# Kernel tuning notes

Hardware: AMD Instinct MI355X
Metric: run time of the kernel (lower is better)

Reference implementation:

```python
import jax, jax.numpy as jnp
import numpy as np

B, S, C = 16, 2048, 1024
H = 8            # preference_dim / num_heads
HD = C // H      # head_dim = 128


def setup_inputs() -> dict:
    key = jax.random.key(0)
    ks = jax.random.split(key, 8)
    s1 = 1.0 / np.sqrt(1.0)   # Linear(1, HD) init scale (not critical)
    sh = 1.0 / np.sqrt(HD)
    return {
        "features": jax.random.normal(ks[0], (B, S, C), dtype=jnp.float32),
        "preference": jax.random.normal(ks[1], (B, H), dtype=jnp.float32),
        "Wq": jax.random.uniform(ks[2], (HD, 1), jnp.float32, -s1, s1),
        "bq": jax.random.uniform(ks[3], (HD,), jnp.float32, -s1, s1),
        "Wk": jax.random.uniform(ks[4], (HD, HD), jnp.float32, -sh, sh),
        "bk": jax.random.uniform(ks[5], (HD,), jnp.float32, -sh, sh),
        "Wv": jax.random.uniform(ks[6], (HD, HD), jnp.float32, -sh, sh),
        "bv": jax.random.uniform(ks[7], (HD,), jnp.float32, -sh, sh),
    }


def reference(features, preference, Wq, bq, Wk, bk, Wv, bv):
    b, s, c = features.shape
    h, hd = H, HD
    # query: Linear(1->hd) applied to per-head scalar preference; constant over step
    # q[b,h,d] = preference[b,h] * Wq[d,0] + bq[d]
    q = preference[:, :, None] * Wq[:, 0][None, None, :] + bq  # [B,H,HD]
    f = features.reshape(b, s, h, hd)                          # head slices
    k = jnp.einsum('bshd,ed->bshe', f, Wk) + bk                # [B,S,H,HD]
    v = jnp.einsum('bshd,ed->bshe', f, Wv) + bv                # [B,S,H,HD]
    # original builds [B,S,S] scores per head, but query rows are identical
    # across step, so softmax(q @ k^T) @ v has identical rows; compute once.
    scores = jnp.einsum('bhd,bshd->bhs', q, k)                 # [B,H,S]
    attn = jax.nn.softmax(scores, axis=-1)
    ctx = jnp.einsum('bhs,bshd->bhd', attn, v)                 # [B,H,HD]
    weighted = jnp.broadcast_to(ctx[:, None, :, :], (b, s, h, hd)).reshape(b, s, c)
    return weighted + features
```

## Files before the change

kernel.cpp:

```cpp
#include <hip/hip_runtime.h>
#include <math.h>

#define B 16
#define S 2048
#define C 1024
#define H 8
#define HD 128

__global__ void k1_qk(const float* __restrict__ pref, const float* __restrict__ Wq,
                      const float* __restrict__ bq, const float* __restrict__ Wk,
                      float* __restrict__ qk) {
    int bh = blockIdx.x;
    int d  = threadIdx.x;
    __shared__ float qsh[HD];
    float p = pref[bh];
    qsh[d] = p * Wq[d] + bq[d];
    __syncthreads();
    float s = 0.f;
#pragma unroll 8
    for (int e = 0; e < HD; ++e)
        s += qsh[e] * Wk[e * HD + d];
    qk[bh * HD + d] = s;
}

__global__ __launch_bounds__(256) void k2_pass(
    const float* __restrict__ feat, const float* __restrict__ qk,
    float* __restrict__ pm, float* __restrict__ pl, float* __restrict__ pf,
    int NC, int R) {
    int wg    = blockIdx.x;
    int b     = wg / NC;
    int chunk = wg - b * NC;
    int t     = threadIdx.x;
    int h     = t >> 5;
    int lane32 = t & 31;

    const float4* frow = (const float4*)feat
                       + (size_t)(b * S + chunk * R) * (C / 4) + t;
    float4 qv = ((const float4*)qk)[(b * H + h) * (HD / 4) + lane32];

    float m = -1e30f, l = 0.f;
    float a0 = 0.f, a1 = 0.f, a2 = 0.f, a3 = 0.f;

    for (int s = 0; s < R; ++s) {
        float4 f = frow[(size_t)s * (C / 4)];
        float part = f.x * qv.x + f.y * qv.y + f.z * qv.z + f.w * qv.w;
        part += __shfl_xor(part, 16, 32);
        part += __shfl_xor(part, 8, 32);
        part += __shfl_xor(part, 4, 32);
        part += __shfl_xor(part, 2, 32);
        part += __shfl_xor(part, 1, 32);
        float mn    = fmaxf(m, part);
        float scale = __expf(m - mn);
        float p     = __expf(part - mn);
        l  = l * scale + p;
        a0 = a0 * scale + p * f.x;
        a1 = a1 * scale + p * f.y;
        a2 = a2 * scale + p * f.z;
        a3 = a3 * scale + p * f.w;
        m  = mn;
    }
    if (lane32 == 0) { pm[wg * H + h] = m; pl[wg * H + h] = l; }
    float4 o; o.x = a0; o.y = a1; o.z = a2; o.w = a3;
    ((float4*)pf)[(size_t)wg * (C / 4) + t] = o;
}

__global__ __launch_bounds__(128) void k3_combine(
    const float* __restrict__ pm, const float* __restrict__ pl,
    const float* __restrict__ pf, const float* __restrict__ Wv,
    const float* __restrict__ bv, float* __restrict__ ctx, int NC) {
    int bh = blockIdx.x;
    int b = bh >> 3, h = bh & 7;
    int t = threadIdx.x;
    __shared__ float wsh[64];
    __shared__ float fsh[HD];

    float M = -1e30f;
    for (int i = 0; i < NC; ++i)
        M = fmaxf(M, pm[(b * NC + i) * H + h]);
    if (t < NC) wsh[t] = __expf(pm[(b * NC + t) * H + h] - M);
    __syncthreads();
    float L = 0.f;
    for (int i = 0; i < NC; ++i)
        L += pl[(b * NC + i) * H + h] * wsh[i];
    float acc = 0.f;
    for (int i = 0; i < NC; ++i)
        acc += pf[(size_t)(b * NC + i) * C + h * HD + t] * wsh[i];
    fsh[t] = acc / L;
    __syncthreads();
    float s = 0.f;
#pragma unroll 8
    for (int d = 0; d < HD; ++d)
        s += fsh[d] * Wv[t * HD + d];
    ctx[bh * HD + t] = s + bv[t];
}

__global__ __launch_bounds__(256) void k4_epilogue(
    const float* __restrict__ feat, const float* __restrict__ ctx,
    float* __restrict__ out) {
    size_t i = (size_t)blockIdx.x * blockDim.x + threadIdx.x;
    float4 f = ((const float4*)feat)[i];
    size_t b  = i >> 19;
    size_t c4 = i & 255;
    float4 cv = ((const float4*)ctx)[b * (C / 4) + c4];
    float4 o; o.x = f.x + cv.x; o.y = f.y + cv.y;
    o.z = f.z + cv.z; o.w = f.w + cv.w;
    ((float4*)out)[i] = o;
}

extern "C" void kernel_launch(void* const* d_in, const int* in_sizes, int n_in,
                              void* d_out, int out_size, void* d_ws, size_t ws_size,
                              hipStream_t stream) {
    const float* feat = (const float*)d_in[0];
    const float* pref = (const float*)d_in[1];
    const float* Wq   = (const float*)d_in[2];
    const float* bq   = (const float*)d_in[3];
    const float* Wk   = (const float*)d_in[4];
    const float* Wv   = (const float*)d_in[6];
    const float* bv   = (const float*)d_in[7];
    float* out = (float*)d_out;

    int NC = 64;
    auto need = [](int nc) {
        return (size_t)(B * H * HD + B * C + 2 * B * nc * H + (size_t)B * nc * C) * 4;
    };
    while (NC > 1 && need(NC) > ws_size) NC >>= 1;
    int R = S / NC;

    float* ws  = (float*)d_ws;
    float* qk  = ws;
    float* ctx = qk + B * H * HD;
    float* pm  = ctx + B * C;
    float* pl  = pm + B * NC * H;
    float* pf  = pl + B * NC * H;

    k1_qk<<<B * H, HD, 0, stream>>>(pref, Wq, bq, Wk, qk);
    k2_pass<<<B * NC, 256, 0, stream>>>(feat, qk, pm, pl, pf, NC, R);
    k3_combine<<<B * H, HD, 0, stream>>>(pm, pl, pf, Wv, bv, ctx, NC);
    k4_epilogue<<<(B * S * C / 4) / 256, 256, 0, stream>>>(feat, ctx, out);
}
```

Baseline: 292.0 us.

## Use lazy max rescaling in online softmax, transpose Wv, nontemporal epilogue stores

The streaming softmax pass now rescales the running max and accumulators only when some lane's score exceeds the current max by more than a threshold, so most iterations need one exp instead of two plus fewer multiplies. Wv is transposed in the first kernel so the combine kernel reads it with coalesced accesses. The epilogue uses a native vector type with nontemporal stores to avoid polluting the cache with the output. The lazy rescale lets exponentials reach up to e^8 relative to the stored max, which narrows the fp32 headroom.

```diff
diff --git a/kernel.cpp b/kernel.cpp
--- a/kernel.cpp
+++ b/kernel.cpp
@@ -7,20 +7,29 @@
 #define H 8
 #define HD 128
 
-__global__ void k1_qk(const float* __restrict__ pref, const float* __restrict__ Wq,
-                      const float* __restrict__ bq, const float* __restrict__ Wk,
-                      float* __restrict__ qk) {
-    int bh = blockIdx.x;
-    int d  = threadIdx.x;
+typedef float f32x4 __attribute__((ext_vector_type(4)));
+
+__global__ __launch_bounds__(128) void k1_qk_tr(
+    const float* __restrict__ pref, const float* __restrict__ Wq,
+    const float* __restrict__ bq, const float* __restrict__ Wk,
+    const float* __restrict__ Wv, float* __restrict__ qk,
+    float* __restrict__ WvT) {
     __shared__ float qsh[HD];
-    float p = pref[bh];
-    qsh[d] = p * Wq[d] + bq[d];
-    __syncthreads();
-    float s = 0.f;
+    int blk = blockIdx.x;
+    int d   = threadIdx.x;
+    if (blk < B * H) {
+        float p = pref[blk];
+        qsh[d] = p * Wq[d] + bq[d];
+        __syncthreads();
+        float s = 0.f;
 #pragma unroll 8
-    for (int e = 0; e < HD; ++e)
-        s += qsh[e] * Wk[e * HD + d];
-    qk[bh * HD + d] = s;
+        for (int e = 0; e < HD; ++e)
+            s += qsh[e] * Wk[e * HD + d];
+        qk[blk * HD + d] = s;
+    } else {
+        int e = blk - B * H;
+        WvT[d * HD + e] = Wv[e * HD + d];
+    }
 }
 
 __global__ __launch_bounds__(256) void k2_pass(
@@ -49,15 +58,18 @@
         part += __shfl_xor(part, 4, 32);
         part += __shfl_xor(part, 2, 32);
         part += __shfl_xor(part, 1, 32);
-        float mn    = fmaxf(m, part);
-        float scale = __expf(m - mn);
-        float p     = __expf(part - mn);
-        l  = l * scale + p;
-        a0 = a0 * scale + p * f.x;
-        a1 = a1 * scale + p * f.y;
-        a2 = a2 * scale + p * f.z;
-        a3 = a3 * scale + p * f.w;
-        m  = mn;
+        if (__any(part - m > 8.f)) {
+            float mn    = fmaxf(m, part);
+            float scale = __expf(m - mn);
+            l *= scale; a0 *= scale; a1 *= scale; a2 *= scale; a3 *= scale;
+            m = mn;
+        }
+        float p = __expf(part - m);
+        l  += p;
+        a0 += p * f.x;
+        a1 += p * f.y;
+        a2 += p * f.z;
+        a3 += p * f.w;
     }
     if (lane32 == 0) { pm[wg * H + h] = m; pl[wg * H + h] = l; }
     float4 o; o.x = a0; o.y = a1; o.z = a2; o.w = a3;
@@ -66,7 +78,7 @@
 
 __global__ __launch_bounds__(128) void k3_combine(
     const float* __restrict__ pm, const float* __restrict__ pl,
-    const float* __restrict__ pf, const float* __restrict__ Wv,
+    const float* __restrict__ pf, const float* __restrict__ WvT,
     const float* __restrict__ bv, float* __restrict__ ctx, int NC) {
     int bh = blockIdx.x;
     int b = bh >> 3, h = bh & 7;
@@ -90,7 +102,7 @@
     float s = 0.f;
 #pragma unroll 8
     for (int d = 0; d < HD; ++d)
-        s += fsh[d] * Wv[t * HD + d];
+        s += fsh[d] * WvT[d * HD + t];
     ctx[bh * HD + t] = s + bv[t];
 }
 
@@ -98,13 +110,12 @@
     const float* __restrict__ feat, const float* __restrict__ ctx,
     float* __restrict__ out) {
     size_t i = (size_t)blockIdx.x * blockDim.x + threadIdx.x;
-    float4 f = ((const float4*)feat)[i];
+    f32x4 f = ((const f32x4*)feat)[i];
     size_t b  = i >> 19;
     size_t c4 = i & 255;
-    float4 cv = ((const float4*)ctx)[b * (C / 4) + c4];
-    float4 o; o.x = f.x + cv.x; o.y = f.y + cv.y;
-    o.z = f.z + cv.z; o.w = f.w + cv.w;
-    ((float4*)out)[i] = o;
+    f32x4 cv = ((const f32x4*)ctx)[b * (C / 4) + c4];
+    f32x4 o = f + cv;
+    __builtin_nontemporal_store(o, &((f32x4*)out)[i]);
 }
 
 extern "C" void kernel_launch(void* const* d_in, const int* in_sizes, int n_in,
@@ -121,7 +132,8 @@
 
     int NC = 64;
     auto need = [](int nc) {
-        return (size_t)(B * H * HD + B * C + 2 * B * nc * H + (size_t)B * nc * C) * 4;
+        return (size_t)(B * H * HD + B * C + HD * HD
+                        + 2 * B * nc * H + (size_t)B * nc * C) * 4;
     };
     while (NC > 1 && need(NC) > ws_size) NC >>= 1;
     int R = S / NC;
@@ -129,12 +141,13 @@
     float* ws  = (float*)d_ws;
     float* qk  = ws;
     float* ctx = qk + B * H * HD;
-    float* pm  = ctx + B * C;
+    float* WvT = ctx + B * C;
+    float* pm  = WvT + HD * HD;
     float* pl  = pm + B * NC * H;
     float* pf  = pl + B * NC * H;
 
-    k1_qk<<<B * H, HD, 0, stream>>>(pref, Wq, bq, Wk, qk);
+    k1_qk_tr<<<B * H + HD, HD, 0, stream>>>(pref, Wq, bq, Wk, Wv, qk, WvT);
     k2_pass<<<B * NC, 256, 0, stream>>>(feat, qk, pm, pl, pf, NC, R);
-    k3_combine<<<B * H, HD, 0, stream>>>(pm, pl, pf, Wv, bv, ctx, NC);
+    k3_combine<<<B * H, HD, 0, stream>>>(pm, pl, pf, WvT, bv, ctx, NC);
     k4_epilogue<<<(B * S * C / 4) / 256, 256, 0, stream>>>(feat, ctx, out);
 }
```

Result: no change. 292.4 us (+0.2%).
